# Performance work log

Hardware: AMD Instinct MI355X
Metric: run time of the kernel (lower is better)

## Reference

```python
import itertools
import jax, jax.numpy as jnp
import numpy as np

N = 400000
CIN, COUT = 32, 64
K, STRIDE, PAD, DIL = 3, 2, 1, 1
SPATIAL = (200, 200, 16)
PRUNING_RATIO = 0.5

def _out_spatial():
    return tuple((s + 2 * PAD - DIL * (K - 1) - 1) // STRIDE + 1 for s in SPATIAL)


def setup_inputs() -> dict:
    key = jax.random.key(0)
    kf, kc0, kc1, kc2, kc3, km, kw = jax.random.split(key, 7)
    features = jax.random.normal(kf, (N, CIN), dtype=jnp.float32)
    b = jax.random.randint(kc0, (N,), 0, 2, dtype=jnp.int32)
    z = jax.random.randint(kc1, (N,), 0, SPATIAL[0], dtype=jnp.int32)
    y = jax.random.randint(kc2, (N,), 0, SPATIAL[1], dtype=jnp.int32)
    x = jax.random.randint(kc3, (N,), 0, SPATIAL[2], dtype=jnp.int32)
    coors = jnp.stack([b, z, y, x], axis=1)  # [N,4] = (batch, d0, d1, d2)
    mask = jax.random.uniform(km, (N,), dtype=jnp.float32)
    weight = jax.random.normal(kw, (K, K, K, CIN, COUT), dtype=jnp.float32) * 0.05
    return {"features": features, "coors": coors, "mask": mask, "weight": weight, "batch_size": 2}


def _sprs_conv(features, coors, mask, weight, batch_size):
    out_sp = _out_spatial()  # (100, 100, 8)
    num_out = batch_size * out_sp[0] * out_sp[1] * out_sp[2]
    n = features.shape[0]
    # rank-based pruning: keep top (1 - pruning_ratio) points as 'important'
    thr = jnp.sort(mask)[int(n * PRUNING_RATIO)]
    important = (mask >= thr)  # [N] bool

    b = coors[:, 0]
    pos = coors[:, 1:4]  # [N,3]
    out_sp_arr = jnp.array(out_sp, dtype=pos.dtype)

    # accumulators; slot num_out is a dump for invalid indices
    acc = jnp.zeros((num_out + 1, COUT), dtype=features.dtype)
    imp_cnt = jnp.zeros((num_out + 1,), dtype=jnp.int32)

    for off in itertools.product(range(K), repeat=3):
        off_arr = jnp.array(off, dtype=pos.dtype)
        num = pos + PAD - DIL * off_arr  # [N,3]
        oc = num // STRIDE
        valid = jnp.all(num % STRIDE == 0, axis=-1) & jnp.all(oc >= 0, axis=-1) & jnp.all(oc < out_sp_arr, axis=-1)
        lin = ((b * out_sp[0] + oc[:, 0]) * out_sp[1] + oc[:, 1]) * out_sp[2] + oc[:, 2]
        idx = jnp.where(valid, lin, num_out)
        vals = features @ weight[off[0], off[1], off[2]]  # [N,Cout] gather-GEMM
        acc = acc.at[idx].add(vals)  # scatter
        imp_cnt = imp_cnt.at[idx].add((important & valid).astype(jnp.int32))

    keep = (imp_cnt[:num_out] > 0)  # output positions reached by >=1 important point
    return acc[:num_out] * keep[:, None]


def reference(features, coors, mask, weight, batch_size):
    return _sprs_conv(features, coors, mask, weight, batch_size)
```

## Files before the change

kernel.cpp:

```cpp
#include <hip/hip_runtime.h>

#define CIN 32
#define COUT 64
#define OD0 100
#define OD1 100
#define OD2 8
#define IZ 200
#define IY 200
#define IX 16
#define NTAP 27
#define NCELLS (2 * IZ * IY * IX)
#define TOY 4
#define TOX 8
#define NROW 27
#define NCELL_R (NROW * 16)
#define CAPB 384


__global__ void hist8_kernel(const float* __restrict__ mask, int n, int level,
                             const int* __restrict__ state, int* __restrict__ hist) {
    __shared__ int h[256];
    h[threadIdx.x] = 0;
    __syncthreads();
    unsigned pfx = level ? (unsigned)state[0] : 0u;
    int sh = 24 - 8 * level;
    for (int i = blockIdx.x * blockDim.x + threadIdx.x; i < n; i += gridDim.x * blockDim.x) {
        unsigned bits = __float_as_uint(mask[i]);
        if (level == 0 || (bits >> (sh + 8)) == pfx)
            atomicAdd(&h[(bits >> sh) & 0xFF], 1);
    }
    __syncthreads();
    int v = h[threadIdx.x];
    if (v) atomicAdd(&hist[threadIdx.x], v);
}

__global__ void select8_kernel(const int* __restrict__ hist, int* __restrict__ state,
                               int level, int rankConst) {
    __shared__ int sc[256];
    sc[threadIdx.x] = hist[threadIdx.x];
    __syncthreads();
    if (threadIdx.x == 0) {
        int rank = level ? state[1] : rankConst;
        unsigned pfx = level ? (unsigned)state[0] : 0u;
        int c = 0;
        for (int j = 0; j < 256; j++) {
            int hv = sc[j];
            if (rank < c + hv) {
                state[0] = (int)((pfx << 8) | (unsigned)j);
                state[1] = rank - c;
                break;
            }
            c += hv;
        }
    }
}


__global__ void transpose_w_kernel(const float* __restrict__ W, float* __restrict__ Wt) {
    int i = blockIdx.x * blockDim.x + threadIdx.x;
    if (i >= NTAP * CIN * COUT) return;
    int cout = i % COUT;
    int rest = i / COUT;
    int cin = rest % CIN;
    int tap = rest / CIN;
    Wt[((size_t)tap * COUT + cout) * CIN + cin] = W[i];
}


__global__ void count_kernel(const int* __restrict__ coors, int n, int* __restrict__ S) {
    int i = blockIdx.x * blockDim.x + threadIdx.x;
    if (i >= n) return;
    const int4 c = ((const int4*)coors)[i];
    int cell = ((c.x * IZ + c.y) * IY + c.z) * IX + c.w;
    atomicAdd(&S[cell], 1);
}

__global__ void scan_l0_kernel(int* __restrict__ S, int* __restrict__ partials) {
    __shared__ int ts[256];
    int tid = threadIdx.x;
    int4 v = ((int4*)S)[blockIdx.x * 256 + tid];
    int s1 = v.x + v.y, s2 = s1 + v.z, s3 = s2 + v.w;
    ts[tid] = s3;
    __syncthreads();
    for (int off = 1; off < 256; off <<= 1) {
        int t = (tid >= off) ? ts[tid - off] : 0;
        __syncthreads();
        ts[tid] += t;
        __syncthreads();
    }
    int excl = ts[tid] - s3;
    int4 o;
    o.x = excl; o.y = excl + v.x; o.z = excl + s1; o.w = excl + s2;
    ((int4*)S)[blockIdx.x * 256 + tid] = o;
    if (tid == 255) partials[blockIdx.x] = ts[255];
}

__global__ void scan_l1_kernel(int* __restrict__ partials, int nP) {
    __shared__ int sums[256];
    int tid = threadIdx.x;
    int per = (nP + 255) / 256;
    int lo = tid * per, hi = lo + per;
    if (hi > nP) hi = nP;
    int s = 0;
    for (int j = lo; j < hi; j++) s += partials[j];
    sums[tid] = s;
    __syncthreads();
    for (int off = 1; off < 256; off <<= 1) {
        int t = (tid >= off) ? sums[tid - off] : 0;
        __syncthreads();
        sums[tid] += t;
        __syncthreads();
    }
    int run = sums[tid] - s;
    for (int j = lo; j < hi; j++) { int v = partials[j]; partials[j] = run; run += v; }
}

__global__ void scan_l2_kernel(int* __restrict__ S, const int* __restrict__ partials) {
    int add = partials[blockIdx.x];
    if (add == 0) return;
    int4 v = ((int4*)S)[blockIdx.x * 256 + threadIdx.x];
    v.x += add; v.y += add; v.z += add; v.w += add;
    ((int4*)S)[blockIdx.x * 256 + threadIdx.x] = v;
}

__global__ void scatter_points_kernel(const int* __restrict__ coors, const float* __restrict__ mask,
                                      const int* __restrict__ state, int n,
                                      int* __restrict__ S, int* __restrict__ entries) {
    int i = blockIdx.x * blockDim.x + threadIdx.x;
    if (i >= n) return;
    const int4 c = ((const int4*)coors)[i];
    int cell = ((c.x * IZ + c.y) * IY + c.z) * IX + c.w;
    float thr = __uint_as_float((unsigned)state[0]);
    int imp = (mask[i] >= thr) ? 1 : 0;
    int pos = atomicAdd(&S[cell], 1);
    entries[pos] = (i << 1) | imp;
}


__global__ void __launch_bounds__(256)
conv_kernel(const float* __restrict__ feat, const float* __restrict__ Wt,
            const int* __restrict__ S, const int* __restrict__ entries,
            float* __restrict__ out) {
    __shared__ float accS[TOY * TOX][COUT];
    __shared__ int   keepS[TOY * TOX];
    __shared__ int   sLds[NROW][17];
    __shared__ unsigned work[6][CAPB];
    __shared__ int   cnt[6];
    __shared__ int   notDone;

    int tid = threadIdx.x;
    int w = tid >> 6;
    int lane = tid & 63;

    int tile = blockIdx.x;
    int oyT = (tile % (OD1 / TOY)) * TOY;
    int rest = tile / (OD1 / TOY);
    int oz = rest % OD0;
    int bb = rest / OD0;

    {
        float4 z = make_float4(0.f, 0.f, 0.f, 0.f);
        float4* a4 = (float4*)&accS[0][0];
        a4[tid] = z;
        a4[tid + 256] = z;
        if (tid < TOY * TOX) keepS[tid] = 0;
    }

    for (int idx = tid; idx < NROW * 17; idx += 256) {
        int row = idx / 17, j = idx % 17;
        int plane = row / 9, pyL = row % 9;
        int pz = 2 * oz - 1 + plane;
        int py = 2 * oyT - 1 + pyL;
        int v = 0;
        if (pz >= 0 && py >= 0) {
            int cellFlat = ((bb * IZ + pz) * IY + py) * IX + (j - 1);
            if (cellFlat >= 0) v = S[cellFlat];
        }
        sLds[row][j] = v;
    }
    __syncthreads();

    int myCl[2]; int nMy = 0;
    for (int cl = tid; cl < NCELL_R; cl += 256) myCl[nMy++] = cl;
    int ci = 0;
    int pi = -1;

    for (;;) {
        if (tid < 6) cnt[tid] = 0;
        if (tid == 0) notDone = 0;
        __syncthreads();

        while (ci < nMy) {
            int cl = myCl[ci];
            int row = cl >> 4, px = cl & 15;
            int rs = (pi < 0) ? sLds[row][px] : pi;
            int re = sLds[row][px + 1];
            int plane = row / 9, pyL = row % 9;
            int bin = plane * 2 + (pyL & 1);
            bool blocked = false;
            for (int i = rs; i < re; i++) {
                int pos = atomicAdd(&cnt[bin], 1);
                if (pos >= CAPB) { pi = i; blocked = true; break; }
                int e = entries[i];
                work[bin][pos] = ((unsigned)(e >> 1) << 9) | (unsigned)((e & 1) << 8)
                               | (unsigned)(pyL << 4) | (unsigned)px;
            }
            if (blocked) break;
            ci++; pi = -1;
        }
        if (ci < nMy) notDone = 1;
        __syncthreads();

        for (int t = w; t < NTAP; t += 4) {
            int o0 = t / 9, r9 = t % 9, o1 = r9 / 3, o2 = r9 % 3;
            int bin = o0 * 2 + (o1 & 1);
            int nb = cnt[bin];
            if (nb > CAPB) nb = CAPB;
            if (nb == 0) continue;

            const float4* wp = (const float4*)(Wt + ((size_t)t * COUT + lane) * CIN);
            float4 w0 = wp[0], w1 = wp[1], w2 = wp[2], w3 = wp[3];
            float4 w4 = wp[4], w5 = wp[5], w6 = wp[6], w7 = wp[7];

            for (int j = 0; j < nb; j++) {
                unsigned e = work[bin][j];
                int pyL = (int)((e >> 4) & 15u);
                int px  = (int)(e & 15u);
                int yy = (pyL - o1) >> 1;
                if ((unsigned)yy >= (unsigned)TOY) continue;
                int dx = px + 1 - o2;
                if (dx & 1) continue;
                int ox = dx >> 1;
                if ((unsigned)ox >= (unsigned)TOX) continue;

                int pid = (int)(e >> 9);
                const float4* fp = (const float4*)(feat + (size_t)pid * CIN);
                float4 f0 = fp[0], f1 = fp[1], f2 = fp[2], f3 = fp[3];
                float4 f4 = fp[4], f5 = fp[5], f6 = fp[6], f7 = fp[7];
                float a0 = 0.f, a1 = 0.f, a2 = 0.f, a3 = 0.f;
                a0 = fmaf(f0.x, w0.x, a0); a0 = fmaf(f0.y, w0.y, a0);
                a0 = fmaf(f0.z, w0.z, a0); a0 = fmaf(f0.w, w0.w, a0);
                a1 = fmaf(f1.x, w1.x, a1); a1 = fmaf(f1.y, w1.y, a1);
                a1 = fmaf(f1.z, w1.z, a1); a1 = fmaf(f1.w, w1.w, a1);
                a2 = fmaf(f2.x, w2.x, a2); a2 = fmaf(f2.y, w2.y, a2);
                a2 = fmaf(f2.z, w2.z, a2); a2 = fmaf(f2.w, w2.w, a2);
                a3 = fmaf(f3.x, w3.x, a3); a3 = fmaf(f3.y, w3.y, a3);
                a3 = fmaf(f3.z, w3.z, a3); a3 = fmaf(f3.w, w3.w, a3);
                a0 = fmaf(f4.x, w4.x, a0); a0 = fmaf(f4.y, w4.y, a0);
                a0 = fmaf(f4.z, w4.z, a0); a0 = fmaf(f4.w, w4.w, a0);
                a1 = fmaf(f5.x, w5.x, a1); a1 = fmaf(f5.y, w5.y, a1);
                a1 = fmaf(f5.z, w5.z, a1); a1 = fmaf(f5.w, w5.w, a1);
                a2 = fmaf(f6.x, w6.x, a2); a2 = fmaf(f6.y, w6.y, a2);
                a2 = fmaf(f6.z, w6.z, a2); a2 = fmaf(f6.w, w6.w, a2);
                a3 = fmaf(f7.x, w7.x, a3); a3 = fmaf(f7.y, w7.y, a3);
                a3 = fmaf(f7.z, w7.z, a3); a3 = fmaf(f7.w, w7.w, a3);

                int cl = yy * TOX + ox;
                atomicAdd(&accS[cl][lane], (a0 + a1) + (a2 + a3));
                if (lane == 0 && (e & 0x100u)) keepS[cl] = 1;
            }
        }
        __syncthreads();
        if (!notDone) break;
    }

#pragma unroll
    for (int k = 0; k < 8; k++) {
        int cl = w * 8 + k;
        int oy = oyT + (cl >> 3);
        int ox = cl & 7;
        size_t cellG = (((size_t)bb * OD0 + oz) * OD1 + oy) * OD2 + ox;
        out[cellG * COUT + lane] = keepS[cl] ? accS[cl][lane] : 0.f;
    }
}


__global__ void __launch_bounds__(256)
scatter_kernel(const float* __restrict__ feat, const int* __restrict__ coors,
               const float* __restrict__ mask, const float* __restrict__ W,
               const int* __restrict__ state, float* __restrict__ out,
               int* __restrict__ keep, int n) {
    int gid = blockIdx.x * blockDim.x + threadIdx.x;
    int wave = gid >> 6;
    int lane = threadIdx.x & 63;
    if (wave >= n) return;

    const int4 c4 = ((const int4*)coors)[wave];
    int bb = c4.x, pz = c4.y, py = c4.z, px = c4.w;

    float thr = __uint_as_float((unsigned)state[0]);
    bool imp = mask[wave] >= thr;

    int oz[2], ozo[2], nz = 0;
    int oy[2], oyo[2], ny = 0;
    int ox[2], oxo[2], nx = 0;
#pragma unroll
    for (int o = 0; o < 3; o++) {
        int num = pz + 1 - o;
        if (num >= 0 && !(num & 1) && (num >> 1) < OD0) { oz[nz] = num >> 1; ozo[nz] = o; nz++; }
        num = py + 1 - o;
        if (num >= 0 && !(num & 1) && (num >> 1) < OD1) { oy[ny] = num >> 1; oyo[ny] = o; ny++; }
        num = px + 1 - o;
        if (num >= 0 && !(num & 1) && (num >> 1) < OD2) { ox[nx] = num >> 1; oxo[nx] = o; nx++; }
    }

    float f[CIN];
    const float4* fp = (const float4*)(feat + (size_t)wave * CIN);
#pragma unroll
    for (int j = 0; j < CIN / 4; j++) {
        float4 v = fp[j];
        f[4 * j + 0] = v.x; f[4 * j + 1] = v.y; f[4 * j + 2] = v.z; f[4 * j + 3] = v.w;
    }

    for (int a = 0; a < nz; a++)
        for (int b = 0; b < ny; b++)
            for (int c = 0; c < nx; c++) {
                int woff = ((ozo[a] * 3 + oyo[b]) * 3 + oxo[c]) * (CIN * COUT);
                const float* wcol = W + woff + lane;
                float acc = 0.f;
#pragma unroll
                for (int k = 0; k < CIN; k++) acc = fmaf(f[k], wcol[k * COUT], acc);
                int lin = ((bb * OD0 + oz[a]) * OD1 + oy[b]) * OD2 + ox[c];
                atomicAdd(out + (size_t)lin * COUT + lane, acc);
                if (imp && lane == 0) keep[lin] = 1;
            }
}

__global__ void finalize_kernel(float* __restrict__ out, const int* __restrict__ keep, int numOut) {
    int t = blockIdx.x * blockDim.x + threadIdx.x;
    if (t >= numOut * (COUT / 4)) return;
    int o = t >> 4;
    if (!keep[o]) ((float4*)out)[t] = make_float4(0.f, 0.f, 0.f, 0.f);
}

extern "C" void kernel_launch(void* const* d_in, const int* in_sizes, int n_in,
                              void* d_out, int out_size, void* d_ws, size_t ws_size,
                              hipStream_t stream) {
    const float* feat  = (const float*)d_in[0];
    const int*   coors = (const int*)d_in[1];
    const float* mask  = (const float*)d_in[2];
    const float* W     = (const float*)d_in[3];

    int n = in_sizes[2];
    int numOut = out_size / COUT;
    int rank = (int)(n * 0.5);

    const int blk = 256;
    int gN = (n + blk - 1) / blk;

    char* ws = (char*)d_ws;

    size_t offHist    = 0;
    size_t offState   = 4 * 256 * 4;
    size_t offS       = offState + 64;
    size_t offPart    = offS + (size_t)NCELLS * 4;
    size_t offEntries = offPart + 1280 * 4;
    size_t offWt      = offEntries + (size_t)n * 4;
    size_t need       = offWt + (size_t)NTAP * CIN * COUT * 4;

    int* hist  = (int*)(ws + offHist);
    int* state = (int*)(ws + offState);

    if (ws_size >= need) {
        int*   S       = (int*)(ws + offS);
        int*   part    = (int*)(ws + offPart);
        int*   entries = (int*)(ws + offEntries);
        float* Wt      = (float*)(ws + offWt);

        hipMemsetAsync(ws, 0, offS + (size_t)NCELLS * 4, stream);

        for (int lvl = 0; lvl < 4; lvl++) {
            hist8_kernel<<<256, blk, 0, stream>>>(mask, n, lvl, state, hist + lvl * 256);
            select8_kernel<<<1, 256, 0, stream>>>(hist + lvl * 256, state, lvl, rank);
        }

        int wElems = NTAP * CIN * COUT;
        transpose_w_kernel<<<(wElems + blk - 1) / blk, blk, 0, stream>>>(W, Wt);

        count_kernel<<<gN, blk, 0, stream>>>(coors, n, S);
        int nBlocksScan = NCELLS / 1024;
        scan_l0_kernel<<<nBlocksScan, 256, 0, stream>>>(S, part);
        scan_l1_kernel<<<1, 256, 0, stream>>>(part, nBlocksScan);
        scan_l2_kernel<<<nBlocksScan, 256, 0, stream>>>(S, part);
        scatter_points_kernel<<<gN, blk, 0, stream>>>(coors, mask, state, n, S, entries);

        int nTiles = numOut / (TOY * TOX);
        conv_kernel<<<nTiles, 256, 0, stream>>>(feat, Wt, S, entries, (float*)d_out);
    } else {
        int* keep = (int*)(ws + offS);
        hipMemsetAsync(d_out, 0, (size_t)out_size * sizeof(float), stream);
        hipMemsetAsync(ws, 0, offS + (size_t)numOut * 4, stream);

        for (int lvl = 0; lvl < 4; lvl++) {
            hist8_kernel<<<256, blk, 0, stream>>>(mask, n, lvl, state, hist + lvl * 256);
            select8_kernel<<<1, 256, 0, stream>>>(hist + lvl * 256, state, lvl, rank);
        }

        long long threads = (long long)n * 64;
        int gScatter = (int)((threads + blk - 1) / blk);
        scatter_kernel<<<gScatter, blk, 0, stream>>>(feat, coors, mask, W, state,
                                                     (float*)d_out, keep, n);

        int fin = numOut * (COUT / 4);
        finalize_kernel<<<(fin + blk - 1) / blk, blk, 0, stream>>>((float*)d_out, keep, numOut);
    }
}
```

Before: 736.1 us.

## Fuse level-0 histogram, count and weight transpose; finish radix select in one block

The first kernel now builds the top-byte histogram of the mask, the per-cell point counts and the transposed weights in a single grid-stride pass. A new single-block, 1024-thread kernel then runs the remaining three radix-select levels, replacing seven separate launches. It compacts candidate mask bits into the entries workspace and then into shared memory to shrink later passes. The aim is to cut launch count and repeated full scans of the mask. The cost is that one block must read all of the mask and do many shared atomics on a single compute unit, which may be slow when the median bucket is large.

```diff
diff --git a/kernel.cpp b/kernel.cpp
--- a/kernel.cpp
+++ b/kernel.cpp
@@ -17,63 +17,128 @@
 #define CAPB 384
 
 
-__global__ void hist8_kernel(const float* __restrict__ mask, int n, int level,
-                             const int* __restrict__ state, int* __restrict__ hist) {
+__global__ void hist0_fused_kernel(const float* __restrict__ mask, const int* __restrict__ coors,
+                                   const float* __restrict__ W, int n,
+                                   int* __restrict__ hist, int* __restrict__ S,
+                                   float* __restrict__ Wt) {
     __shared__ int h[256];
     h[threadIdx.x] = 0;
     __syncthreads();
-    unsigned pfx = level ? (unsigned)state[0] : 0u;
-    int sh = 24 - 8 * level;
     for (int i = blockIdx.x * blockDim.x + threadIdx.x; i < n; i += gridDim.x * blockDim.x) {
         unsigned bits = __float_as_uint(mask[i]);
-        if (level == 0 || (bits >> (sh + 8)) == pfx)
-            atomicAdd(&h[(bits >> sh) & 0xFF], 1);
+        atomicAdd(&h[bits >> 24], 1);
+        const int4 c = ((const int4*)coors)[i];
+        atomicAdd(&S[((c.x * IZ + c.y) * IY + c.z) * IX + c.w], 1);
+    }
+    for (int i = blockIdx.x * blockDim.x + threadIdx.x; i < NTAP * CIN * COUT;
+         i += gridDim.x * blockDim.x) {
+        int cout = i % COUT;
+        int rest = i / COUT;
+        int cin = rest % CIN;
+        int tap = rest / CIN;
+        Wt[((size_t)tap * COUT + cout) * CIN + cin] = W[i];
     }
     __syncthreads();
     int v = h[threadIdx.x];
     if (v) atomicAdd(&hist[threadIdx.x], v);
 }
 
-__global__ void select8_kernel(const int* __restrict__ hist, int* __restrict__ state,
-                               int level, int rankConst) {
-    __shared__ int sc[256];
-    sc[threadIdx.x] = hist[threadIdx.x];
-    __syncthreads();
-    if (threadIdx.x == 0) {
-        int rank = level ? state[1] : rankConst;
-        unsigned pfx = level ? (unsigned)state[0] : 0u;
+
+__global__ void __launch_bounds__(1024)
+sel4_kernel(const float* __restrict__ mask, int n, const int* __restrict__ hist0,
+            int rank0, int* __restrict__ state, unsigned* __restrict__ scratch) {
+    __shared__ int h[256];
+    __shared__ int cand[4096];
+    __shared__ int scnt;
+    __shared__ int sel;
+    __shared__ int rnk;
+    int tid = threadIdx.x;
+
+    if (tid == 0) {
         int c = 0;
         for (int j = 0; j < 256; j++) {
-            int hv = sc[j];
-            if (rank < c + hv) {
-                state[0] = (int)((pfx << 8) | (unsigned)j);
-                state[1] = rank - c;
-                break;
-            }
+            int hv = hist0[j];
+            if (rank0 < c + hv) { sel = j; rnk = rank0 - c; break; }
             c += hv;
         }
     }
-}
-
-
-__global__ void transpose_w_kernel(const float* __restrict__ W, float* __restrict__ Wt) {
-    int i = blockIdx.x * blockDim.x + threadIdx.x;
-    if (i >= NTAP * CIN * COUT) return;
-    int cout = i % COUT;
-    int rest = i / COUT;
-    int cin = rest % CIN;
-    int tap = rest / CIN;
-    Wt[((size_t)tap * COUT + cout) * CIN + cin] = W[i];
-}
-
-
-__global__ void count_kernel(const int* __restrict__ coors, int n, int* __restrict__ S) {
-    int i = blockIdx.x * blockDim.x + threadIdx.x;
-    if (i >= n) return;
-    const int4 c = ((const int4*)coors)[i];
-    int cell = ((c.x * IZ + c.y) * IY + c.z) * IX + c.w;
-    atomicAdd(&S[cell], 1);
-}
+    __syncthreads();
+    if (tid < 256) h[tid] = 0;
+    if (tid == 0) scnt = 0;
+    __syncthreads();
+    unsigned p0 = (unsigned)sel;
+
+    for (int i = tid; i < n; i += 1024) {
+        unsigned bits = __float_as_uint(mask[i]);
+        if ((bits >> 24) == p0) {
+            atomicAdd(&h[(bits >> 16) & 0xFF], 1);
+            int pos = atomicAdd(&scnt, 1);
+            scratch[pos] = bits;
+        }
+    }
+    __syncthreads();
+    int nScratch = scnt;
+    if (tid == 0) {
+        int c = 0, r = rnk;
+        for (int j = 0; j < 256; j++) {
+            int hv = h[j];
+            if (r < c + hv) { sel = (sel << 8) | j; rnk = r - c; break; }
+            c += hv;
+        }
+    }
+    __syncthreads();
+    if (tid < 256) h[tid] = 0;
+    if (tid == 0) scnt = 0;
+    __syncthreads();
+    unsigned p1 = (unsigned)sel;
+
+    for (int i = tid; i < nScratch; i += 1024) {
+        unsigned bits = scratch[i];
+        if ((bits >> 16) == p1) {
+            atomicAdd(&h[(bits >> 8) & 0xFF], 1);
+            int pos = atomicAdd(&scnt, 1);
+            if (pos < 4096) cand[pos] = (int)bits;
+        }
+    }
+    __syncthreads();
+    int nCand = scnt;
+    bool useLds = (nCand <= 4096);
+    if (tid == 0) {
+        int c = 0, r = rnk;
+        for (int j = 0; j < 256; j++) {
+            int hv = h[j];
+            if (r < c + hv) { sel = (sel << 8) | j; rnk = r - c; break; }
+            c += hv;
+        }
+    }
+    __syncthreads();
+    if (tid < 256) h[tid] = 0;
+    __syncthreads();
+    unsigned p2 = (unsigned)sel;
+
+    if (useLds) {
+        for (int i = tid; i < nCand; i += 1024) {
+            unsigned bits = (unsigned)cand[i];
+            if ((bits >> 8) == p2) atomicAdd(&h[bits & 0xFF], 1);
+        }
+    } else {
+        for (int i = tid; i < nScratch; i += 1024) {
+            unsigned bits = scratch[i];
+            if ((bits >> 8) == p2) atomicAdd(&h[bits & 0xFF], 1);
+        }
+    }
+    __syncthreads();
+    if (tid == 0) {
+        int c = 0, r = rnk;
+        for (int j = 0; j < 256; j++) {
+            int hv = h[j];
+            if (r < c + hv) { sel = (sel << 8) | j; break; }
+            c += hv;
+        }
+        state[0] = sel;
+    }
+}
+
 
 __global__ void scan_l0_kernel(int* __restrict__ S, int* __restrict__ partials) {
     __shared__ int ts[256];
@@ -275,6 +340,57 @@
 }
 
 
+__global__ void hist0_simple_kernel(const float* __restrict__ mask, int n, int* __restrict__ hist) {
+    __shared__ int h[256];
+    h[threadIdx.x] = 0;
+    __syncthreads();
+    for (int i = blockIdx.x * blockDim.x + threadIdx.x; i < n; i += gridDim.x * blockDim.x) {
+        unsigned bits = __float_as_uint(mask[i]);
+        atomicAdd(&h[bits >> 24], 1);
+    }
+    __syncthreads();
+    int v = h[threadIdx.x];
+    if (v) atomicAdd(&hist[threadIdx.x], v);
+}
+
+__global__ void hist8_kernel(const float* __restrict__ mask, int n, int level,
+                             const int* __restrict__ state, int* __restrict__ hist) {
+    __shared__ int h[256];
+    h[threadIdx.x] = 0;
+    __syncthreads();
+    unsigned pfx = (unsigned)state[0];
+    int sh = 24 - 8 * level;
+    for (int i = blockIdx.x * blockDim.x + threadIdx.x; i < n; i += gridDim.x * blockDim.x) {
+        unsigned bits = __float_as_uint(mask[i]);
+        if ((bits >> (sh + 8)) == pfx)
+            atomicAdd(&h[(bits >> sh) & 0xFF], 1);
+    }
+    __syncthreads();
+    int v = h[threadIdx.x];
+    if (v) atomicAdd(&hist[threadIdx.x], v);
+}
+
+__global__ void select8_kernel(const int* __restrict__ hist, int* __restrict__ state,
+                               int level, int rankConst) {
+    __shared__ int sc[256];
+    sc[threadIdx.x] = hist[threadIdx.x];
+    __syncthreads();
+    if (threadIdx.x == 0) {
+        int rank = level ? state[1] : rankConst;
+        unsigned pfx = level ? (unsigned)state[0] : 0u;
+        int c = 0;
+        for (int j = 0; j < 256; j++) {
+            int hv = sc[j];
+            if (rank < c + hv) {
+                state[0] = (int)((pfx << 8) | (unsigned)j);
+                state[1] = rank - c;
+                break;
+            }
+            c += hv;
+        }
+    }
+}
+
 __global__ void __launch_bounds__(256)
 scatter_kernel(const float* __restrict__ feat, const int* __restrict__ coors,
                const float* __restrict__ mask, const float* __restrict__ W,
@@ -333,6 +449,7 @@
     if (!keep[o]) ((float4*)out)[t] = make_float4(0.f, 0.f, 0.f, 0.f);
 }
 
+
 extern "C" void kernel_launch(void* const* d_in, const int* in_sizes, int n_in,
                               void* d_out, int out_size, void* d_ws, size_t ws_size,
                               hipStream_t stream) {
@@ -369,15 +486,9 @@
 
         hipMemsetAsync(ws, 0, offS + (size_t)NCELLS * 4, stream);
 
-        for (int lvl = 0; lvl < 4; lvl++) {
-            hist8_kernel<<<256, blk, 0, stream>>>(mask, n, lvl, state, hist + lvl * 256);
-            select8_kernel<<<1, 256, 0, stream>>>(hist + lvl * 256, state, lvl, rank);
-        }
-
-        int wElems = NTAP * CIN * COUT;
-        transpose_w_kernel<<<(wElems + blk - 1) / blk, blk, 0, stream>>>(W, Wt);
-
-        count_kernel<<<gN, blk, 0, stream>>>(coors, n, S);
+        hist0_fused_kernel<<<256, blk, 0, stream>>>(mask, coors, W, n, hist, S, Wt);
+        sel4_kernel<<<1, 1024, 0, stream>>>(mask, n, hist, rank, state, (unsigned*)entries);
+
         int nBlocksScan = NCELLS / 1024;
         scan_l0_kernel<<<nBlocksScan, 256, 0, stream>>>(S, part);
         scan_l1_kernel<<<1, 256, 0, stream>>>(part, nBlocksScan);
@@ -391,7 +502,9 @@
         hipMemsetAsync(d_out, 0, (size_t)out_size * sizeof(float), stream);
         hipMemsetAsync(ws, 0, offS + (size_t)numOut * 4, stream);
 
-        for (int lvl = 0; lvl < 4; lvl++) {
+        hist0_simple_kernel<<<256, blk, 0, stream>>>(mask, n, hist);
+        select8_kernel<<<1, 256, 0, stream>>>(hist, state, 0, rank);
+        for (int lvl = 1; lvl < 4; lvl++) {
             hist8_kernel<<<256, blk, 0, stream>>>(mask, n, lvl, state, hist + lvl * 256);
             select8_kernel<<<1, 256, 0, stream>>>(hist + lvl * 256, state, lvl, rank);
         }
```

New measurement: 922.1 us. 25.3% more time.

## Fuse first histogram pass with point counting and weight transpose; software-pipeline feature loads

Applied to the files above, without the earlier changes.

Merges the level-0 radix histogram, the per-cell point count and the weight transpose into one grid-stride kernel. This drops two launches and shares one pass over the points. In the conv inner loop, the next point's features are now loaded before the previous point's dot product and shared-memory atomic run, so gather latency overlaps with compute. The cost is higher register pressure from holding two feature sets, and the fused kernel runs with only 256 blocks for the count atomics.

```diff
diff --git a/kernel.cpp b/kernel.cpp
--- a/kernel.cpp
+++ b/kernel.cpp
@@ -17,16 +17,43 @@
 #define CAPB 384
 
 
+__global__ void hist0_fused_kernel(const float* __restrict__ mask, const int* __restrict__ coors,
+                                   const float* __restrict__ W, int n,
+                                   int* __restrict__ hist, int* __restrict__ S,
+                                   float* __restrict__ Wt) {
+    __shared__ int h[256];
+    h[threadIdx.x] = 0;
+    __syncthreads();
+    for (int i = blockIdx.x * blockDim.x + threadIdx.x; i < n; i += gridDim.x * blockDim.x) {
+        unsigned bits = __float_as_uint(mask[i]);
+        atomicAdd(&h[bits >> 24], 1);
+        const int4 c = ((const int4*)coors)[i];
+        atomicAdd(&S[((c.x * IZ + c.y) * IY + c.z) * IX + c.w], 1);
+    }
+    for (int i = blockIdx.x * blockDim.x + threadIdx.x; i < NTAP * CIN * COUT;
+         i += gridDim.x * blockDim.x) {
+        int cout = i % COUT;
+        int rest = i / COUT;
+        int cin = rest % CIN;
+        int tap = rest / CIN;
+        Wt[((size_t)tap * COUT + cout) * CIN + cin] = W[i];
+    }
+    __syncthreads();
+    int v = h[threadIdx.x];
+    if (v) atomicAdd(&hist[threadIdx.x], v);
+}
+
+
 __global__ void hist8_kernel(const float* __restrict__ mask, int n, int level,
                              const int* __restrict__ state, int* __restrict__ hist) {
     __shared__ int h[256];
     h[threadIdx.x] = 0;
     __syncthreads();
-    unsigned pfx = level ? (unsigned)state[0] : 0u;
+    unsigned pfx = (unsigned)state[0];
     int sh = 24 - 8 * level;
     for (int i = blockIdx.x * blockDim.x + threadIdx.x; i < n; i += gridDim.x * blockDim.x) {
         unsigned bits = __float_as_uint(mask[i]);
-        if (level == 0 || (bits >> (sh + 8)) == pfx)
+        if ((bits >> (sh + 8)) == pfx)
             atomicAdd(&h[(bits >> sh) & 0xFF], 1);
     }
     __syncthreads();
@@ -55,25 +82,6 @@
     }
 }
 
-
-__global__ void transpose_w_kernel(const float* __restrict__ W, float* __restrict__ Wt) {
-    int i = blockIdx.x * blockDim.x + threadIdx.x;
-    if (i >= NTAP * CIN * COUT) return;
-    int cout = i % COUT;
-    int rest = i / COUT;
-    int cin = rest % CIN;
-    int tap = rest / CIN;
-    Wt[((size_t)tap * COUT + cout) * CIN + cin] = W[i];
-}
-
-
-__global__ void count_kernel(const int* __restrict__ coors, int n, int* __restrict__ S) {
-    int i = blockIdx.x * blockDim.x + threadIdx.x;
-    if (i >= n) return;
-    const int4 c = ((const int4*)coors)[i];
-    int cell = ((c.x * IZ + c.y) * IY + c.z) * IX + c.w;
-    atomicAdd(&S[cell], 1);
-}
 
 __global__ void scan_l0_kernel(int* __restrict__ S, int* __restrict__ partials) {
     __shared__ int ts[256];
@@ -222,6 +230,9 @@
             float4 w0 = wp[0], w1 = wp[1], w2 = wp[2], w3 = wp[3];
             float4 w4 = wp[4], w5 = wp[5], w6 = wp[6], w7 = wp[7];
 
+            int pcl = -1;
+            float4 f0, f1, f2, f3, f4, f5, f6, f7;
+
             for (int j = 0; j < nb; j++) {
                 unsigned e = work[bin][j];
                 int pyL = (int)((e >> 4) & 15u);
@@ -235,8 +246,37 @@
 
                 int pid = (int)(e >> 9);
                 const float4* fp = (const float4*)(feat + (size_t)pid * CIN);
-                float4 f0 = fp[0], f1 = fp[1], f2 = fp[2], f3 = fp[3];
-                float4 f4 = fp[4], f5 = fp[5], f6 = fp[6], f7 = fp[7];
+                float4 n0 = fp[0], n1 = fp[1], n2 = fp[2], n3 = fp[3];
+                float4 n4 = fp[4], n5 = fp[5], n6 = fp[6], n7 = fp[7];
+
+                if (pcl >= 0) {
+                    float a0 = 0.f, a1 = 0.f, a2 = 0.f, a3 = 0.f;
+                    a0 = fmaf(f0.x, w0.x, a0); a0 = fmaf(f0.y, w0.y, a0);
+                    a0 = fmaf(f0.z, w0.z, a0); a0 = fmaf(f0.w, w0.w, a0);
+                    a1 = fmaf(f1.x, w1.x, a1); a1 = fmaf(f1.y, w1.y, a1);
+                    a1 = fmaf(f1.z, w1.z, a1); a1 = fmaf(f1.w, w1.w, a1);
+                    a2 = fmaf(f2.x, w2.x, a2); a2 = fmaf(f2.y, w2.y, a2);
+                    a2 = fmaf(f2.z, w2.z, a2); a2 = fmaf(f2.w, w2.w, a2);
+                    a3 = fmaf(f3.x, w3.x, a3); a3 = fmaf(f3.y, w3.y, a3);
+                    a3 = fmaf(f3.z, w3.z, a3); a3 = fmaf(f3.w, w3.w, a3);
+                    a0 = fmaf(f4.x, w4.x, a0); a0 = fmaf(f4.y, w4.y, a0);
+                    a0 = fmaf(f4.z, w4.z, a0); a0 = fmaf(f4.w, w4.w, a0);
+                    a1 = fmaf(f5.x, w5.x, a1); a1 = fmaf(f5.y, w5.y, a1);
+                    a1 = fmaf(f5.z, w5.z, a1); a1 = fmaf(f5.w, w5.w, a1);
+                    a2 = fmaf(f6.x, w6.x, a2); a2 = fmaf(f6.y, w6.y, a2);
+                    a2 = fmaf(f6.z, w6.z, a2); a2 = fmaf(f6.w, w6.w, a2);
+                    a3 = fmaf(f7.x, w7.x, a3); a3 = fmaf(f7.y, w7.y, a3);
+                    a3 = fmaf(f7.z, w7.z, a3); a3 = fmaf(f7.w, w7.w, a3);
+                    atomicAdd(&accS[pcl][lane], (a0 + a1) + (a2 + a3));
+                }
+
+                f0 = n0; f1 = n1; f2 = n2; f3 = n3;
+                f4 = n4; f5 = n5; f6 = n6; f7 = n7;
+                pcl = yy * TOX + ox;
+                if (lane == 0 && (e & 0x100u)) keepS[pcl] = 1;
+            }
+
+            if (pcl >= 0) {
                 float a0 = 0.f, a1 = 0.f, a2 = 0.f, a3 = 0.f;
                 a0 = fmaf(f0.x, w0.x, a0); a0 = fmaf(f0.y, w0.y, a0);
                 a0 = fmaf(f0.z, w0.z, a0); a0 = fmaf(f0.w, w0.w, a0);
@@ -254,10 +294,7 @@
                 a2 = fmaf(f6.z, w6.z, a2); a2 = fmaf(f6.w, w6.w, a2);
                 a3 = fmaf(f7.x, w7.x, a3); a3 = fmaf(f7.y, w7.y, a3);
                 a3 = fmaf(f7.z, w7.z, a3); a3 = fmaf(f7.w, w7.w, a3);
-
-                int cl = yy * TOX + ox;
-                atomicAdd(&accS[cl][lane], (a0 + a1) + (a2 + a3));
-                if (lane == 0 && (e & 0x100u)) keepS[cl] = 1;
+                atomicAdd(&accS[pcl][lane], (a0 + a1) + (a2 + a3));
             }
         }
         __syncthreads();
@@ -274,6 +311,19 @@
     }
 }
 
+
+__global__ void hist0_simple_kernel(const float* __restrict__ mask, int n, int* __restrict__ hist) {
+    __shared__ int h[256];
+    h[threadIdx.x] = 0;
+    __syncthreads();
+    for (int i = blockIdx.x * blockDim.x + threadIdx.x; i < n; i += gridDim.x * blockDim.x) {
+        unsigned bits = __float_as_uint(mask[i]);
+        atomicAdd(&h[bits >> 24], 1);
+    }
+    __syncthreads();
+    int v = h[threadIdx.x];
+    if (v) atomicAdd(&hist[threadIdx.x], v);
+}
 
 __global__ void __launch_bounds__(256)
 scatter_kernel(const float* __restrict__ feat, const int* __restrict__ coors,
@@ -333,6 +383,7 @@
     if (!keep[o]) ((float4*)out)[t] = make_float4(0.f, 0.f, 0.f, 0.f);
 }
 
+
 extern "C" void kernel_launch(void* const* d_in, const int* in_sizes, int n_in,
                               void* d_out, int out_size, void* d_ws, size_t ws_size,
                               hipStream_t stream) {
@@ -369,15 +420,13 @@
 
         hipMemsetAsync(ws, 0, offS + (size_t)NCELLS * 4, stream);
 
-        for (int lvl = 0; lvl < 4; lvl++) {
+        hist0_fused_kernel<<<256, blk, 0, stream>>>(mask, coors, W, n, hist, S, Wt);
+        select8_kernel<<<1, 256, 0, stream>>>(hist, state, 0, rank);
+        for (int lvl = 1; lvl < 4; lvl++) {
             hist8_kernel<<<256, blk, 0, stream>>>(mask, n, lvl, state, hist + lvl * 256);
             select8_kernel<<<1, 256, 0, stream>>>(hist + lvl * 256, state, lvl, rank);
         }
 
-        int wElems = NTAP * CIN * COUT;
-        transpose_w_kernel<<<(wElems + blk - 1) / blk, blk, 0, stream>>>(W, Wt);
-
-        count_kernel<<<gN, blk, 0, stream>>>(coors, n, S);
         int nBlocksScan = NCELLS / 1024;
         scan_l0_kernel<<<nBlocksScan, 256, 0, stream>>>(S, part);
         scan_l1_kernel<<<1, 256, 0, stream>>>(part, nBlocksScan);
@@ -391,7 +440,9 @@
         hipMemsetAsync(d_out, 0, (size_t)out_size * sizeof(float), stream);
         hipMemsetAsync(ws, 0, offS + (size_t)numOut * 4, stream);
 
-        for (int lvl = 0; lvl < 4; lvl++) {
+        hist0_simple_kernel<<<256, blk, 0, stream>>>(mask, n, hist);
+        select8_kernel<<<1, 256, 0, stream>>>(hist, state, 0, rank);
+        for (int lvl = 1; lvl < 4; lvl++) {
             hist8_kernel<<<256, blk, 0, stream>>>(mask, n, lvl, state, hist + lvl * 256);
             select8_kernel<<<1, 256, 0, stream>>>(hist + lvl * 256, state, lvl, rank);
         }
```

Result: no change. 733.6 us (-0.3%).
